# Kernel tuning notes

Measured on AMD Instinct MI355X. Metric: run time of the kernel, lower is better.

Reference implementation:

```python
import jax, jax.numpy as jnp
import numpy as np


def conv1x1(x, w, b):
    # x: [B,C,H,W], w: [O,C], b: [O]
    return jnp.einsum('oc,bchw->bohw', w, x) + b[None, :, None, None]


def interp_bilinear_ac(x, oh, ow):
    # bilinear resize with align_corners=True, x: [B,C,H,W] -> [B,C,oh,ow]
    B, C, H, W = x.shape
    if (H, W) == (oh, ow):
        return x
    ys = jnp.linspace(0.0, H - 1.0, oh)
    xs = jnp.linspace(0.0, W - 1.0, ow)
    y0 = jnp.clip(jnp.floor(ys).astype(jnp.int32), 0, H - 1)
    y1 = jnp.minimum(y0 + 1, H - 1)
    x0 = jnp.clip(jnp.floor(xs).astype(jnp.int32), 0, W - 1)
    x1 = jnp.minimum(x0 + 1, W - 1)
    wy = (ys - y0).astype(x.dtype)
    wx = (xs - x0).astype(x.dtype)
    top = x[:, :, y0, :] * (1 - wy)[None, None, :, None] + x[:, :, y1, :] * wy[None, None, :, None]
    out = top[:, :, :, x0] * (1 - wx)[None, None, None, :] + top[:, :, :, x1] * wx[None, None, None, :]
    return out


def non_local(x, qw, qb, kw, kb, vw, vb, ow_, ob):
    B, C, H, W = x.shape
    HW = H * W
    q = conv1x1(x, qw, qb).reshape(B, -1, HW)  # [B, Ci, HW]
    k = conv1x1(x, kw, kb).reshape(B, -1, HW)
    v = conv1x1(x, vw, vb).reshape(B, -1, HW)
    attn = jnp.einsum('bci,bcj->bij', q, k)     # [B, HW, HW]
    attn = jax.nn.softmax(attn, axis=-1)
    out = jnp.einsum('bcj,bij->bci', v, attn)   # [B, Ci, HW]
    out = out.reshape(B, -1, H, W)
    return conv1x1(out, ow_, ob)


def _forward(x1, x2, x3, x4, qw, qb, kw, kb, vw, vb, ow_, ob, g1w, g1b, g2w, g2b):
    H1, W1 = x1.shape[2], x1.shape[3]
    x2_up = interp_bilinear_ac(x2, H1, W1)
    x3_up = interp_bilinear_ac(x3, H1, W1)
    x4_up = interp_bilinear_ac(x4, H1, W1)
    gf = jnp.concatenate([x1, x2_up, x3_up, x4_up], axis=1)  # [B, 128, H1, W1]
    gf = non_local(gf, qw, qb, kw, kb, vw, vb, ow_, ob)
    h = jax.nn.relu(conv1x1(gf, g1w, g1b))
    sw = jax.nn.sigmoid(conv1x1(h, g2w, g2b))                # [B, 128, H1, W1]
    w1, w2, w3, w4 = sw[:, :32], sw[:, 32:64], sw[:, 64:96], sw[:, 96:128]
    x1_out = x1 * (1 + w1)
    x2_out = x2 * (1 + interp_bilinear_ac(w2, x2.shape[2], x2.shape[3]))
    x3_out = x3 * (1 + interp_bilinear_ac(w3, x3.shape[2], x3.shape[3]))
    x4_out = x4 * (1 + interp_bilinear_ac(w4, x4.shape[2], x4.shape[3]))
    return (x1_out, x2_out, x3_out, x4_out)


def setup_inputs() -> dict:
    key = jax.random.key(0)
    ks = jax.random.split(key, 16)
    C = 128  # channel*4
    Ci = 64  # inter_channel
    Cg = 32
    d = {
        'x1': jax.random.normal(ks[0], (8, 32, 64, 64), jnp.float32),
        'x2': jax.random.normal(ks[1], (8, 32, 32, 32), jnp.float32),
        'x3': jax.random.normal(ks[2], (8, 32, 16, 16), jnp.float32),
        'x4': jax.random.normal(ks[3], (8, 32, 8, 8), jnp.float32),
        'qw': jax.random.normal(ks[4], (Ci, C), jnp.float32) * 0.05,
        'qb': jnp.zeros((Ci,), jnp.float32),
        'kw': jax.random.normal(ks[5], (Ci, C), jnp.float32) * 0.05,
        'kb': jnp.zeros((Ci,), jnp.float32),
        'vw': jax.random.normal(ks[6], (Ci, C), jnp.float32) * 0.05,
        'vb': jnp.zeros((Ci,), jnp.float32),
        'ow_': jax.random.normal(ks[7], (C, Ci), jnp.float32) * 0.05,
        'ob': jnp.zeros((C,), jnp.float32),
        'g1w': jax.random.normal(ks[8], (Cg, C), jnp.float32) * 0.05,
        'g1b': jnp.zeros((Cg,), jnp.float32),
        'g2w': jax.random.normal(ks[9], (C, Cg), jnp.float32) * 0.05,
        'g2b': jnp.zeros((C,), jnp.float32),
    }
    return d


def reference(x1, x2, x3, x4, qw, qb, kw, kb, vw, vb, ow_, ob, g1w, g1b, g2w, g2b):
    return _forward(x1, x2, x3, x4, qw, qb, kw, kb, vw, vb, ow_, ob, g1w, g1b, g2w, g2b)
```

## Files before the change

kernel.cpp:

```cpp
#include <hip/hip_runtime.h>
#include <hip/hip_bf16.h>


typedef __attribute__((ext_vector_type(8))) short s16x8;
typedef __attribute__((ext_vector_type(4))) float f32x4;
typedef __attribute__((ext_vector_type(16))) float f32x16;

#define LOG2E 1.44269504088896340736f

__device__ __forceinline__ unsigned int f2bf(float f) {
    unsigned int u = __float_as_uint(f);
    u += 0x7fffu + ((u >> 16) & 1u);
    return u >> 16;
}
__device__ __forceinline__ unsigned int pk2bf(float a, float b) {
    union { __hip_bfloat162 h; unsigned int u; } cv;
    cv.h = __float22bfloat162_rn(make_float2(a, b));
    return cv.u;
}
__device__ __forceinline__ float bf2f(unsigned short u) {
    return __uint_as_float((unsigned int)u << 16);
}
__device__ __forceinline__ float fexp2(float x) { return __builtin_amdgcn_exp2f(x); }
__device__ __forceinline__ float frcp(float x)  { return __builtin_amdgcn_rcpf(x); }
__device__ __forceinline__ s16x8 cvt8(const float* __restrict__ p, float scale) {
    float4 a = ((const float4*)p)[0];
    float4 b = ((const float4*)p)[1];
    union { s16x8 v; uint4 u; } cv;
    cv.u.x = pk2bf(a.x * scale, a.y * scale);
    cv.u.y = pk2bf(a.z * scale, a.w * scale);
    cv.u.z = pk2bf(b.x * scale, b.y * scale);
    cv.u.w = pk2bf(b.z * scale, b.w * scale);
    return cv.v;
}

__global__ __launch_bounds__(256, 4) void k_qkv(
    const float* __restrict__ x1, const float* __restrict__ x2,
    const float* __restrict__ x3, const float* __restrict__ x4,
    const float* __restrict__ qw, const float* __restrict__ qb,
    const float* __restrict__ kw, const float* __restrict__ kb,
    const float* __restrict__ vw, const float* __restrict__ vb,
    unsigned short* __restrict__ Qg, unsigned short* __restrict__ Kg,
    unsigned short* __restrict__ Vg) {
  __shared__ __align__(16) unsigned short gfb[32 * 136];
  unsigned int* gfbu = (unsigned int*)gfb;

  const int blk = blockIdx.x;
  const int b = blk >> 7;
  const int i0 = (blk & 127) << 5;
  const int t = threadIdx.x;
  const int wv = t >> 6, lane = t & 63;
  const int r = lane & 15, qd = lane >> 4;
  f32x4 zf = {0.f, 0.f, 0.f, 0.f};

  {
    const int cp = t >> 2, q = t & 3;
    const int c0 = cp << 1;
    const int pbase = q << 3;
    const int oy = i0 >> 6;
    const int ox0 = (i0 & 63) | (q << 3);

    if (cp < 16) {
      const float* s0 = x1 + (((b * 32 + c0) << 12) + (oy << 6) + ox0);
      const float* s1 = s0 + 4096;
      #pragma unroll
      for (int k4 = 0; k4 < 2; k4++) {
        float4 va = ((const float4*)s0)[k4];
        float4 vb = ((const float4*)s1)[k4];
        int p = pbase + k4 * 4;
        gfbu[(p + 0) * 68 + cp] = pk2bf(va.x, vb.x);
        gfbu[(p + 1) * 68 + cp] = pk2bf(va.y, vb.y);
        gfbu[(p + 2) * 68 + cp] = pk2bf(va.z, vb.z);
        gfbu[(p + 3) * 68 + cp] = pk2bf(va.w, vb.w);
      }
    } else {
      const float* base; int S, cs;
      if (cp < 32)      { base = x2; S = 32; cs = c0 - 32; }
      else if (cp < 48) { base = x3; S = 16; cs = c0 - 64; }
      else              { base = x4; S = 8;  cs = c0 - 96; }
      const float* pl0 = base + (b * 32 + cs) * S * S;
      const float* pl1 = pl0 + S * S;
      float yf = (float)oy * (float)(S - 1) * (1.0f / 63.0f);
      int y0 = (int)yf; if (y0 > S - 1) y0 = S - 1;
      int y1 = y0 + 1;  if (y1 > S - 1) y1 = S - 1;
      float wy = yf - (float)y0;
      const float* r00 = pl0 + y0 * S; const float* r01 = pl0 + y1 * S;
      const float* r10 = pl1 + y0 * S; const float* r11 = pl1 + y1 * S;
      for (int k = 0; k < 8; k++) {
        int ox = ox0 + k;
        float xf = (float)ox * (float)(S - 1) * (1.0f / 63.0f);
        int xx0 = (int)xf; if (xx0 > S - 1) xx0 = S - 1;
        int xx1 = xx0 + 1; if (xx1 > S - 1) xx1 = S - 1;
        float wx = xf - (float)xx0;
        float a0 = r00[xx0] + wx * (r00[xx1] - r00[xx0]);
        float b0 = r01[xx0] + wx * (r01[xx1] - r01[xx0]);
        float v0 = a0 + wy * (b0 - a0);
        float a1 = r10[xx0] + wx * (r10[xx1] - r10[xx0]);
        float b1 = r11[xx0] + wx * (r11[xx1] - r11[xx0]);
        float v1 = a1 + wy * (b1 - a1);
        gfbu[(pbase + k) * 68 + cp] = pk2bf(v0, v1);
      }
    }
  }
  __syncthreads();

  const int ocb = wv * 48;
  s16x8 af[3][4];
  float4 bias[3];
  #pragma unroll
  for (int mti = 0; mti < 3; mti++) {
    const int goc = ocb + mti * 16;
    const float* wsrc; const float* bsrc; float scale;
    if (goc < 64)       { wsrc = qw + goc * 128;         bsrc = qb + goc;         scale = LOG2E; }
    else if (goc < 128) { wsrc = kw + (goc - 64) * 128;  bsrc = kb + (goc - 64);  scale = 1.0f; }
    else                { wsrc = vw + (goc - 128) * 128; bsrc = vb + (goc - 128); scale = 1.0f; }
    #pragma unroll
    for (int ks = 0; ks < 4; ks++)
      af[mti][ks] = cvt8(wsrc + r * 128 + ks * 32 + qd * 8, scale);
    float4 bv = *(const float4*)(bsrc + qd * 4);
    bias[mti] = make_float4(bv.x * scale, bv.y * scale, bv.z * scale, bv.w * scale);
  }

  #pragma unroll
  for (int nt = 0; nt < 2; nt++) {
    s16x8 bfr[4];
    #pragma unroll
    for (int ks = 0; ks < 4; ks++)
      bfr[ks] = *(const s16x8*)&gfb[(nt * 16 + r) * 136 + ks * 32 + qd * 8];
    f32x4 acc[3] = {zf, zf, zf};
    #pragma unroll
    for (int ks = 0; ks < 4; ks++)
      #pragma unroll
      for (int mti = 0; mti < 3; mti++)
        acc[mti] = __builtin_amdgcn_mfma_f32_16x16x32_bf16(af[mti][ks], bfr[ks], acc[mti], 0, 0, 0);

    const int pos = i0 + nt * 16 + r;
    #pragma unroll
    for (int mti = 0; mti < 3; mti++) {
      const int gmt = wv * 3 + mti;
      float ax = acc[mti].x + bias[mti].x;
      float ay = acc[mti].y + bias[mti].y;
      float az = acc[mti].z + bias[mti].z;
      float aw = acc[mti].w + bias[mti].w;
      if (gmt < 4) {
        uint2 w; w.x = pk2bf(ax, ay); w.y = pk2bf(az, aw);
        *(uint2*)&Qg[(((b << 12) + pos) << 6) + gmt * 16 + qd * 4] = w;
      } else if (gmt < 8) {
        uint2 w; w.x = pk2bf(ax, ay); w.y = pk2bf(az, aw);
        *(uint2*)&Kg[(((b << 12) + pos) << 6) + (gmt - 4) * 16 + qd * 4] = w;
      } else {
        int ocv = (gmt - 8) * 16 + qd * 4;
        Vg[((b * 64 + ocv + 0) << 12) + pos] = (unsigned short)f2bf(ax);
        Vg[((b * 64 + ocv + 1) << 12) + pos] = (unsigned short)f2bf(ay);
        Vg[((b * 64 + ocv + 2) << 12) + pos] = (unsigned short)f2bf(az);
        Vg[((b * 64 + ocv + 3) << 12) + pos] = (unsigned short)f2bf(aw);
      }
    }
  }
}

__global__ __launch_bounds__(256, 4) void k_attn(
    const unsigned short* __restrict__ Qg, const unsigned short* __restrict__ Kg,
    const unsigned short* __restrict__ Vg, unsigned short* __restrict__ Op,
    float* __restrict__ Lp) {
  __shared__ __align__(16) unsigned short Kl[64 * 72];
  __shared__ __align__(16) unsigned short Vl[64 * 72];

  const int b = blockIdx.x >> 7;
  const int part = (blockIdx.x >> 5) & 3;
  const int qg = blockIdx.x & 31;
  const int i0 = qg << 7;
  const int t = threadIdx.x;
  const int wv = t >> 6, lane = t & 63;
  const int q = lane & 31, hi = lane >> 5;
  const int qbase = i0 + wv * 32;

  s16x8 qf[4];
  #pragma unroll
  for (int kc = 0; kc < 4; kc++)
    qf[kc] = *(const s16x8*)&Qg[(((b << 12) + qbase + q) << 6) + kc * 16 + hi * 8];

  f32x16 acc[2];
  #pragma unroll
  for (int m = 0; m < 2; m++)
    #pragma unroll
    for (int e = 0; e < 16; e++) acc[m][e] = 0.f;
  float ls = 0.f;

  const int srow = t >> 3, sseg = t & 7;
  const unsigned short* kt0 = &Kg[(((b << 12) + (part << 10) + srow) << 6) + sseg * 8];
  const unsigned short* vt0 = &Vg[((b * 64 + srow) << 12) + (part << 10) + sseg * 8];
  uint4 pk0 = *(const uint4*)(kt0);
  uint4 pk1 = *(const uint4*)(kt0 + (32 << 6));
  uint4 pv0 = *(const uint4*)(vt0);
  uint4 pv1 = *(const uint4*)(vt0 + (32 << 12));

  for (int it = 0; it < 16; it++) {
    __syncthreads();
    *(uint4*)&Kl[srow * 72 + sseg * 8] = pk0;
    *(uint4*)&Kl[(srow + 32) * 72 + sseg * 8] = pk1;
    *(uint4*)&Vl[srow * 72 + sseg * 8] = pv0;
    *(uint4*)&Vl[(srow + 32) * 72 + sseg * 8] = pv1;
    __syncthreads();
    if (it < 15) {
      int j0 = (it + 1) << 6;
      pk0 = *(const uint4*)(kt0 + (j0 << 6));
      pk1 = *(const uint4*)(kt0 + ((j0 + 32) << 6));
      pv0 = *(const uint4*)(vt0 + j0);
      pv1 = *(const uint4*)(vt0 + (32 << 12) + j0);
    }

    unsigned int pu[2][8];
    #pragma unroll
    for (int kt = 0; kt < 2; kt++) {
      f32x16 st;
      #pragma unroll
      for (int e = 0; e < 16; e++) st[e] = 0.f;
      #pragma unroll
      for (int kc = 0; kc < 4; kc++) {
        s16x8 kf = *(const s16x8*)&Kl[(kt * 32 + q) * 72 + kc * 16 + hi * 8];
        st = __builtin_amdgcn_mfma_f32_32x32x16_bf16(kf, qf[kc], st, 0, 0, 0);
      }
      float lsum = 0.f;
      #pragma unroll
      for (int i2 = 0; i2 < 8; i2++) {
        float p0 = fexp2(st[2 * i2]);
        float p1 = fexp2(st[2 * i2 + 1]);
        lsum += p0 + p1;
        pu[kt][i2] = pk2bf(p0, p1);
      }
      ls += lsum;
    }

    #pragma unroll
    for (int kt = 0; kt < 2; kt++) {
      #pragma unroll
      for (int c16 = 0; c16 < 2; c16++) {
        const int c16g = kt * 2 + c16;
        unsigned int a0 = pu[kt][c16 * 4 + 0], a1 = pu[kt][c16 * 4 + 1];
        unsigned int a2 = pu[kt][c16 * 4 + 2], a3 = pu[kt][c16 * 4 + 3];
        unsigned int k0 = hi ? a2 : a0, k1 = hi ? a3 : a1;
        unsigned int s0 = hi ? a0 : a2, s1 = hi ? a1 : a3;
        unsigned int r0 = __shfl_xor(s0, 32);
        unsigned int r1 = __shfl_xor(s1, 32);
        union { s16x8 v; unsigned int u[4]; } pb;
        pb.u[0] = hi ? r0 : k0;
        pb.u[1] = hi ? r1 : k1;
        pb.u[2] = hi ? k0 : r0;
        pb.u[3] = hi ? k1 : r1;
        #pragma unroll
        for (int mtv = 0; mtv < 2; mtv++) {
          s16x8 vf = *(const s16x8*)&Vl[(mtv * 32 + q) * 72 + c16g * 16 + hi * 8];
          acc[mtv] = __builtin_amdgcn_mfma_f32_32x32x16_bf16(vf, pb.v, acc[mtv], 0, 0, 0);
        }
      }
    }
  }

  ls += __shfl_xor(ls, 32);
  float inv = frcp(ls);
  const int qrow = qbase + q;
  unsigned short* orow = &Op[(((part * 8 + b) << 12) + qrow) << 6];
  #pragma unroll
  for (int mtv = 0; mtv < 2; mtv++) {
    #pragma unroll
    for (int i2 = 0; i2 < 8; i2++) {
      int dbase = ((2 * i2) & 3) + 8 * ((2 * i2) >> 2) + 4 * hi + mtv * 32;
      *(unsigned int*)&orow[dbase] =
          pk2bf(acc[mtv][2 * i2] * inv, acc[mtv][2 * i2 + 1] * inv);
    }
  }
  if (hi == 0) Lp[((part * 8 + b) << 12) + qrow] = ls;
}

__global__ __launch_bounds__(256, 4) void k_out(
    const unsigned short* __restrict__ Op, const float* __restrict__ Lp,
    const float* __restrict__ ow, const float* __restrict__ obias,
    const float* __restrict__ g1w, const float* __restrict__ g1b,
    const float* __restrict__ g2w, const float* __restrict__ g2b,
    const float* __restrict__ x1, float* __restrict__ out,
    unsigned short* __restrict__ SWb) {
  __shared__ __align__(16) unsigned short Ot[32 * 72];
  __shared__ __align__(16) unsigned short gf2t[32 * 136];
  __shared__ __align__(16) unsigned short ht[32 * 40];
  const int blk = blockIdx.x;
  const int b = blk >> 7;
  const int i0 = (blk & 127) << 5;
  const int t = threadIdx.x;
  const int wv = t >> 6, lane = t & 63;
  const int r = lane & 15, qd = lane >> 4;
  f32x4 zf = {0.f, 0.f, 0.f, 0.f};

  {
    const int pos = t >> 3, seg = t & 7;
    const int i = i0 + pos;
    float lp4[4], lsum = 0.f;
    #pragma unroll
    for (int p = 0; p < 4; p++) { lp4[p] = Lp[((p * 8 + b) << 12) + i]; lsum += lp4[p]; }
    float o[8];
    #pragma unroll
    for (int k = 0; k < 8; k++) o[k] = 0.f;
    float invs = frcp(lsum);
    #pragma unroll
    for (int p = 0; p < 4; p++) {
      float w = lp4[p] * invs;
      uint4 u = *(const uint4*)&Op[((((p * 8 + b) << 12) + i) << 6) + seg * 8];
      o[0] += w * __uint_as_float(u.x << 16);
      o[1] += w * __uint_as_float(u.x & 0xFFFF0000u);
      o[2] += w * __uint_as_float(u.y << 16);
      o[3] += w * __uint_as_float(u.y & 0xFFFF0000u);
      o[4] += w * __uint_as_float(u.z << 16);
      o[5] += w * __uint_as_float(u.z & 0xFFFF0000u);
      o[6] += w * __uint_as_float(u.w << 16);
      o[7] += w * __uint_as_float(u.w & 0xFFFF0000u);
    }
    unsigned int* dst = (unsigned int*)&Ot[pos * 72 + seg * 8];
    #pragma unroll
    for (int k = 0; k < 4; k++) dst[k] = pk2bf(o[2 * k], o[2 * k + 1]);
  }
  __syncthreads();

  {
    const int ocb = wv * 32;
    s16x8 af[2][2];
    #pragma unroll
    for (int mt = 0; mt < 2; mt++)
      #pragma unroll
      for (int ks = 0; ks < 2; ks++)
        af[mt][ks] = cvt8(&ow[(ocb + mt * 16 + r) * 64 + ks * 32 + qd * 8], 1.0f);
    float4 bias[2];
    #pragma unroll
    for (int mt = 0; mt < 2; mt++)
      bias[mt] = *(const float4*)&obias[ocb + mt * 16 + qd * 4];
    #pragma unroll
    for (int nt = 0; nt < 2; nt++) {
      s16x8 bfr[2];
      #pragma unroll
      for (int ks = 0; ks < 2; ks++)
        bfr[ks] = *(const s16x8*)&Ot[(nt * 16 + r) * 72 + ks * 32 + qd * 8];
      f32x4 acc[2] = {zf, zf};
      #pragma unroll
      for (int ks = 0; ks < 2; ks++)
        #pragma unroll
        for (int mt = 0; mt < 2; mt++)
          acc[mt] = __builtin_amdgcn_mfma_f32_16x16x32_bf16(af[mt][ks], bfr[ks], acc[mt], 0, 0, 0);
      #pragma unroll
      for (int mt = 0; mt < 2; mt++) {
        uint2 w;
        w.x = pk2bf(acc[mt].x + bias[mt].x, acc[mt].y + bias[mt].y);
        w.y = pk2bf(acc[mt].z + bias[mt].z, acc[mt].w + bias[mt].w);
        *(uint2*)&gf2t[(nt * 16 + r) * 136 + ocb + mt * 16 + qd * 4] = w;
      }
    }
  }
  __syncthreads();

  {
    const int mt = wv & 1, pt = wv >> 1;
    s16x8 af[4];
    #pragma unroll
    for (int ks = 0; ks < 4; ks++)
      af[ks] = cvt8(&g1w[(mt * 16 + r) * 128 + ks * 32 + qd * 8], 1.0f);
    float4 bias = *(const float4*)&g1b[mt * 16 + qd * 4];
    s16x8 bfr[4];
    #pragma unroll
    for (int ks = 0; ks < 4; ks++)
      bfr[ks] = *(const s16x8*)&gf2t[(pt * 16 + r) * 136 + ks * 32 + qd * 8];
    f32x4 acc = zf;
    #pragma unroll
    for (int ks = 0; ks < 4; ks++)
      acc = __builtin_amdgcn_mfma_f32_16x16x32_bf16(af[ks], bfr[ks], acc, 0, 0, 0);
    uint2 w;
    w.x = pk2bf(fmaxf(acc.x + bias.x, 0.f), fmaxf(acc.y + bias.y, 0.f));
    w.y = pk2bf(fmaxf(acc.z + bias.z, 0.f), fmaxf(acc.w + bias.w, 0.f));
    *(uint2*)&ht[(pt * 16 + r) * 40 + mt * 16 + qd * 4] = w;
  }
  __syncthreads();

  {
    const int nb = wv * 32;
    s16x8 bfg[2];
    float bias[2];
    #pragma unroll
    for (int ntl = 0; ntl < 2; ntl++) {
      bfg[ntl] = cvt8(&g2w[(nb + ntl * 16 + r) * 32 + qd * 8], 1.0f);
      bias[ntl] = g2b[nb + ntl * 16 + r];
    }
    #pragma unroll
    for (int mt = 0; mt < 2; mt++) {
      s16x8 af = *(const s16x8*)&ht[(mt * 16 + r) * 40 + qd * 8];
      #pragma unroll
      for (int ntl = 0; ntl < 2; ntl++) {
        f32x4 acc = __builtin_amdgcn_mfma_f32_16x16x32_bf16(af, bfg[ntl], zf, 0, 0, 0);
        const int oc3 = nb + ntl * 16 + r;
        float s0 = frcp(1.0f + fexp2(-LOG2E * (acc.x + bias[ntl])));
        float s1 = frcp(1.0f + fexp2(-LOG2E * (acc.y + bias[ntl])));
        float s2 = frcp(1.0f + fexp2(-LOG2E * (acc.z + bias[ntl])));
        float s3 = frcp(1.0f + fexp2(-LOG2E * (acc.w + bias[ntl])));
        if (nb == 0) {
          const int off = ((b * 32 + oc3) << 12) + i0 + mt * 16 + qd * 4;
          float4 xv = *(const float4*)&x1[off];
          float4 o4;
          o4.x = xv.x * (1.f + s0); o4.y = xv.y * (1.f + s1);
          o4.z = xv.z * (1.f + s2); o4.w = xv.w * (1.f + s3);
          *(float4*)&out[off] = o4;
        } else {
          uint2 w; w.x = pk2bf(s0, s1); w.y = pk2bf(s2, s3);
          *(uint2*)&SWb[((b * 128 + oc3) << 12) + i0 + mt * 16 + qd * 4] = w;
        }
      }
    }
  }
}

__device__ __forceinline__ float bilin64(const unsigned short* __restrict__ p,
                                         int oy, int ox, int n) {
  float yf = (float)oy * 63.0f / (float)n;
  int y0 = (int)yf; if (y0 > 63) y0 = 63;
  int y1 = y0 + 1;  if (y1 > 63) y1 = 63;
  float wy = yf - (float)y0;
  float xf = (float)ox * 63.0f / (float)n;
  int x0 = (int)xf; if (x0 > 63) x0 = 63;
  int x1 = x0 + 1;  if (x1 > 63) x1 = 63;
  float wx = xf - (float)x0;
  float v00 = bf2f(p[y0 * 64 + x0]), v01 = bf2f(p[y0 * 64 + x1]);
  float v10 = bf2f(p[y1 * 64 + x0]), v11 = bf2f(p[y1 * 64 + x1]);
  float top = v00 + wx * (v01 - v00);
  float bot = v10 + wx * (v11 - v10);
  return top + wy * (bot - top);
}

__global__ __launch_bounds__(256) void k_final(
    const float* __restrict__ x2, const float* __restrict__ x3,
    const float* __restrict__ x4,
    const unsigned short* __restrict__ SWb, float* __restrict__ out) {
  const int N1 = 1048576, N2 = 262144, N3 = 65536, N4 = 16384;
  int idx = blockIdx.x * 256 + threadIdx.x;
  if (idx < N2) {
    int b = idx >> 15, rr = idx & 32767;
    int c = rr >> 10, oy = (rr >> 5) & 31, ox = rr & 31;
    float w = bilin64(SWb + ((b * 128 + 32 + c) << 12), oy, ox, 31);
    out[N1 + idx] = x2[idx] * (1.f + w);
  } else if (idx < N2 + N3) {
    int i3 = idx - N2;
    int b = i3 >> 13, rr = i3 & 8191;
    int c = rr >> 8, oy = (rr >> 4) & 15, ox = rr & 15;
    float w = bilin64(SWb + ((b * 128 + 64 + c) << 12), oy, ox, 15);
    out[N1 + idx] = x3[i3] * (1.f + w);
  } else if (idx < N2 + N3 + N4) {
    int i4 = idx - N2 - N3;
    int b = i4 >> 11, rr = i4 & 2047;
    int c = rr >> 6, oy = (rr >> 3) & 7, ox = rr & 7;
    float w = bilin64(SWb + ((b * 128 + 96 + c) << 12), oy, ox, 7);
    out[N1 + idx] = x4[i4] * (1.f + w);
  }
}

extern "C" void kernel_launch(void* const* d_in, const int* in_sizes, int n_in,
                              void* d_out, int out_size, void* d_ws, size_t ws_size,
                              hipStream_t stream) {
  const float* x1  = (const float*)d_in[0];
  const float* x2  = (const float*)d_in[1];
  const float* x3  = (const float*)d_in[2];
  const float* x4  = (const float*)d_in[3];
  const float* qw  = (const float*)d_in[4];
  const float* qb  = (const float*)d_in[5];
  const float* kw  = (const float*)d_in[6];
  const float* kb  = (const float*)d_in[7];
  const float* vw  = (const float*)d_in[8];
  const float* vb  = (const float*)d_in[9];
  const float* ow  = (const float*)d_in[10];
  const float* ob  = (const float*)d_in[11];
  const float* g1w = (const float*)d_in[12];
  const float* g1b = (const float*)d_in[13];
  const float* g2w = (const float*)d_in[14];
  const float* g2b = (const float*)d_in[15];
  float* out = (float*)d_out;

  char* ws = (char*)d_ws;
  unsigned short* Qg  = (unsigned short*)(ws + 0);
  unsigned short* Kg  = (unsigned short*)(ws + 4194304);
  unsigned short* Vg  = (unsigned short*)(ws + 8388608);
  unsigned short* SWb = (unsigned short*)(ws + 0);
  unsigned short* Op  = (unsigned short*)(ws + 12582912);
  float* Lp   = (float*)(ws + 29360128);

  k_qkv<<<1024, 256, 0, stream>>>(x1, x2, x3, x4, qw, qb, kw, kb, vw, vb,
                                  Qg, Kg, Vg);
  k_attn<<<1024, 256, 0, stream>>>(Qg, Kg, Vg, Op, Lp);
  k_out<<<1024, 256, 0, stream>>>(Op, Lp, ow, ob, g1w, g1b, g2w, g2b,
                                  x1, out, SWb);
  k_final<<<1344, 256, 0, stream>>>(x2, x3, x4, SWb, out);
}
```

Before: 183.7 us.

## Pre-convert weights to bf16 in a prep kernel and double-buffer attention LDS tiles

Adds a small prep kernel that converts all 1x1 conv weights to bf16 once, with the log2e scale folded into Q weights and bias. The QKV and output kernels then load the packed bf16 directly instead of converting fp32 per block. The attention kernel double-buffers its K/V shared-memory tiles, which removes one barrier per iteration. This costs an extra kernel launch and doubles LDS use in the attention kernel, which may reduce occupancy.

```diff
diff --git a/kernel.cpp b/kernel.cpp
--- a/kernel.cpp
+++ b/kernel.cpp
@@ -23,23 +23,41 @@
 }
 __device__ __forceinline__ float fexp2(float x) { return __builtin_amdgcn_exp2f(x); }
 __device__ __forceinline__ float frcp(float x)  { return __builtin_amdgcn_rcpf(x); }
-__device__ __forceinline__ s16x8 cvt8(const float* __restrict__ p, float scale) {
-    float4 a = ((const float4*)p)[0];
-    float4 b = ((const float4*)p)[1];
-    union { s16x8 v; uint4 u; } cv;
-    cv.u.x = pk2bf(a.x * scale, a.y * scale);
-    cv.u.y = pk2bf(a.z * scale, a.w * scale);
-    cv.u.z = pk2bf(b.x * scale, b.y * scale);
-    cv.u.w = pk2bf(b.z * scale, b.w * scale);
-    return cv.v;
+
+__global__ __launch_bounds__(256) void k_prep(
+    const float* __restrict__ qw, const float* __restrict__ qb,
+    const float* __restrict__ kw, const float* __restrict__ kb,
+    const float* __restrict__ vw, const float* __restrict__ vb,
+    const float* __restrict__ ow, const float* __restrict__ g1w,
+    const float* __restrict__ g2w,
+    unsigned short* __restrict__ WTb, float* __restrict__ bqkv,
+    unsigned short* __restrict__ owb, unsigned short* __restrict__ g1wb,
+    unsigned short* __restrict__ g2wb) {
+  int t = blockIdx.x * 256 + threadIdx.x;
+  if (t < 192 * 128) {
+    int oc = t >> 7, c = t & 127;
+    float v;
+    if (oc < 64)       v = qw[oc * 128 + c] * LOG2E;
+    else if (oc < 128) v = kw[(oc - 64) * 128 + c];
+    else               v = vw[(oc - 128) * 128 + c];
+    WTb[t] = (unsigned short)f2bf(v);
+  }
+  if (t < 192) {
+    float v;
+    if (t < 64)       v = qb[t] * LOG2E;
+    else if (t < 128) v = kb[t - 64];
+    else              v = vb[t - 128];
+    bqkv[t] = v;
+  }
+  if (t < 128 * 64) owb[t]  = (unsigned short)f2bf(ow[t]);
+  if (t < 32 * 128) g1wb[t] = (unsigned short)f2bf(g1w[t]);
+  if (t < 128 * 32) g2wb[t] = (unsigned short)f2bf(g2w[t]);
 }
 
 __global__ __launch_bounds__(256, 4) void k_qkv(
     const float* __restrict__ x1, const float* __restrict__ x2,
     const float* __restrict__ x3, const float* __restrict__ x4,
-    const float* __restrict__ qw, const float* __restrict__ qb,
-    const float* __restrict__ kw, const float* __restrict__ kb,
-    const float* __restrict__ vw, const float* __restrict__ vb,
+    const unsigned short* __restrict__ WTb, const float* __restrict__ bqkv,
     unsigned short* __restrict__ Qg, unsigned short* __restrict__ Kg,
     unsigned short* __restrict__ Vg) {
   __shared__ __align__(16) unsigned short gfb[32 * 136];
@@ -109,16 +127,10 @@
   float4 bias[3];
   #pragma unroll
   for (int mti = 0; mti < 3; mti++) {
-    const int goc = ocb + mti * 16;
-    const float* wsrc; const float* bsrc; float scale;
-    if (goc < 64)       { wsrc = qw + goc * 128;         bsrc = qb + goc;         scale = LOG2E; }
-    else if (goc < 128) { wsrc = kw + (goc - 64) * 128;  bsrc = kb + (goc - 64);  scale = 1.0f; }
-    else                { wsrc = vw + (goc - 128) * 128; bsrc = vb + (goc - 128); scale = 1.0f; }
     #pragma unroll
     for (int ks = 0; ks < 4; ks++)
-      af[mti][ks] = cvt8(wsrc + r * 128 + ks * 32 + qd * 8, scale);
-    float4 bv = *(const float4*)(bsrc + qd * 4);
-    bias[mti] = make_float4(bv.x * scale, bv.y * scale, bv.z * scale, bv.w * scale);
+      af[mti][ks] = *(const s16x8*)&WTb[(ocb + mti * 16 + r) * 128 + ks * 32 + qd * 8];
+    bias[mti] = *(const float4*)&bqkv[ocb + mti * 16 + qd * 4];
   }
 
   #pragma unroll
@@ -163,8 +175,8 @@
     const unsigned short* __restrict__ Qg, const unsigned short* __restrict__ Kg,
     const unsigned short* __restrict__ Vg, unsigned short* __restrict__ Op,
     float* __restrict__ Lp) {
-  __shared__ __align__(16) unsigned short Kl[64 * 72];
-  __shared__ __align__(16) unsigned short Vl[64 * 72];
+  __shared__ __align__(16) unsigned short Kl[2][64 * 72];
+  __shared__ __align__(16) unsigned short Vl[2][64 * 72];
 
   const int b = blockIdx.x >> 7;
   const int part = (blockIdx.x >> 5) & 3;
@@ -196,11 +208,12 @@
   uint4 pv1 = *(const uint4*)(vt0 + (32 << 12));
 
   for (int it = 0; it < 16; it++) {
-    __syncthreads();
-    *(uint4*)&Kl[srow * 72 + sseg * 8] = pk0;
-    *(uint4*)&Kl[(srow + 32) * 72 + sseg * 8] = pk1;
-    *(uint4*)&Vl[srow * 72 + sseg * 8] = pv0;
-    *(uint4*)&Vl[(srow + 32) * 72 + sseg * 8] = pv1;
+    unsigned short* Kb = Kl[it & 1];
+    unsigned short* Vb = Vl[it & 1];
+    *(uint4*)&Kb[srow * 72 + sseg * 8] = pk0;
+    *(uint4*)&Kb[(srow + 32) * 72 + sseg * 8] = pk1;
+    *(uint4*)&Vb[srow * 72 + sseg * 8] = pv0;
+    *(uint4*)&Vb[(srow + 32) * 72 + sseg * 8] = pv1;
     __syncthreads();
     if (it < 15) {
       int j0 = (it + 1) << 6;
@@ -218,7 +231,7 @@
       for (int e = 0; e < 16; e++) st[e] = 0.f;
       #pragma unroll
       for (int kc = 0; kc < 4; kc++) {
-        s16x8 kf = *(const s16x8*)&Kl[(kt * 32 + q) * 72 + kc * 16 + hi * 8];
+        s16x8 kf = *(const s16x8*)&Kb[(kt * 32 + q) * 72 + kc * 16 + hi * 8];
         st = __builtin_amdgcn_mfma_f32_32x32x16_bf16(kf, qf[kc], st, 0, 0, 0);
       }
       float lsum = 0.f;
@@ -250,7 +263,7 @@
         pb.u[3] = hi ? k1 : r1;
         #pragma unroll
         for (int mtv = 0; mtv < 2; mtv++) {
-          s16x8 vf = *(const s16x8*)&Vl[(mtv * 32 + q) * 72 + c16g * 16 + hi * 8];
+          s16x8 vf = *(const s16x8*)&Vb[(mtv * 32 + q) * 72 + c16g * 16 + hi * 8];
           acc[mtv] = __builtin_amdgcn_mfma_f32_32x32x16_bf16(vf, pb.v, acc[mtv], 0, 0, 0);
         }
       }
@@ -275,9 +288,9 @@
 
 __global__ __launch_bounds__(256, 4) void k_out(
     const unsigned short* __restrict__ Op, const float* __restrict__ Lp,
-    const float* __restrict__ ow, const float* __restrict__ obias,
-    const float* __restrict__ g1w, const float* __restrict__ g1b,
-    const float* __restrict__ g2w, const float* __restrict__ g2b,
+    const unsigned short* __restrict__ owb, const float* __restrict__ obias,
+    const unsigned short* __restrict__ g1wb, const float* __restrict__ g1b,
+    const unsigned short* __restrict__ g2wb, const float* __restrict__ g2b,
     const float* __restrict__ x1, float* __restrict__ out,
     unsigned short* __restrict__ SWb) {
   __shared__ __align__(16) unsigned short Ot[32 * 72];
@@ -327,7 +340,7 @@
     for (int mt = 0; mt < 2; mt++)
       #pragma unroll
       for (int ks = 0; ks < 2; ks++)
-        af[mt][ks] = cvt8(&ow[(ocb + mt * 16 + r) * 64 + ks * 32 + qd * 8], 1.0f);
+        af[mt][ks] = *(const s16x8*)&owb[(ocb + mt * 16 + r) * 64 + ks * 32 + qd * 8];
     float4 bias[2];
     #pragma unroll
     for (int mt = 0; mt < 2; mt++)
@@ -360,7 +373,7 @@
     s16x8 af[4];
     #pragma unroll
     for (int ks = 0; ks < 4; ks++)
-      af[ks] = cvt8(&g1w[(mt * 16 + r) * 128 + ks * 32 + qd * 8], 1.0f);
+      af[ks] = *(const s16x8*)&g1wb[(mt * 16 + r) * 128 + ks * 32 + qd * 8];
     float4 bias = *(const float4*)&g1b[mt * 16 + qd * 4];
     s16x8 bfr[4];
     #pragma unroll
@@ -383,7 +396,7 @@
     float bias[2];
     #pragma unroll
     for (int ntl = 0; ntl < 2; ntl++) {
-      bfg[ntl] = cvt8(&g2w[(nb + ntl * 16 + r) * 32 + qd * 8], 1.0f);
+      bfg[ntl] = *(const s16x8*)&g2wb[(nb + ntl * 16 + r) * 32 + qd * 8];
       bias[ntl] = g2b[nb + ntl * 16 + r];
     }
     #pragma unroll
@@ -484,11 +497,17 @@
   unsigned short* SWb = (unsigned short*)(ws + 0);
   unsigned short* Op  = (unsigned short*)(ws + 12582912);
   float* Lp   = (float*)(ws + 29360128);
-
-  k_qkv<<<1024, 256, 0, stream>>>(x1, x2, x3, x4, qw, qb, kw, kb, vw, vb,
-                                  Qg, Kg, Vg);
+  unsigned short* WTb = (unsigned short*)(ws + 29884416);
+  float* bqkv = (float*)(ws + 29933568);
+  unsigned short* owb  = (unsigned short*)(ws + 29934592);
+  unsigned short* g1wb = (unsigned short*)(ws + 29950976);
+  unsigned short* g2wb = (unsigned short*)(ws + 29959168);
+
+  k_prep<<<96, 256, 0, stream>>>(qw, qb, kw, kb, vw, vb, ow, g1w, g2w,
+                                 WTb, bqkv, owb, g1wb, g2wb);
+  k_qkv<<<1024, 256, 0, stream>>>(x1, x2, x3, x4, WTb, bqkv, Qg, Kg, Vg);
   k_attn<<<1024, 256, 0, stream>>>(Qg, Kg, Vg, Op, Lp);
-  k_out<<<1024, 256, 0, stream>>>(Op, Lp, ow, ob, g1w, g1b, g2w, g2b,
+  k_out<<<1024, 256, 0, stream>>>(Op, Lp, owb, ob, g1wb, g1b, g2wb, g2b,
                                   x1, out, SWb);
   k_final<<<1344, 256, 0, stream>>>(x2, x3, x4, SWb, out);
 }
```

Result: faster. 173.8 us (-5.4%).
